# Optimization experiments

Measured on AMD Instinct MI355X. Metric: run time of the kernel, lower is better.

## Reference

```python
import jax, jax.numpy as jnp
import numpy as np


def _conv1d(x, w, pad):
    # torch F.conv1d is cross-correlation; so is lax.conv_general_dilated.
    # x: (k, c_in, N), w: (c_out, c_in, K) -> (k, c_out, N + 2*pad - K + 1)
    return jax.lax.conv_general_dilated(
        x, w, window_strides=(1,), padding=[(pad, pad)],
        dimension_numbers=("NCH", "OIH", "NCH"))


def setup_inputs() -> dict:
    key = jax.random.key(0)
    k1, k2, k3, k4, k5 = jax.random.split(key, 5)
    k_b, c_out, c_in, N, m = 4, 64, 8, 4096, 8
    z_real = jax.random.normal(k1, (k_b, c_in, N), dtype=jnp.float32)
    z_imag = jax.random.normal(k2, (k_b, c_in, N), dtype=jnp.float32)
    A = jax.random.uniform(k3, (c_out, c_in, 1), jnp.float32, 0.75, 1.25)
    beta = jax.random.uniform(k4, (c_out, c_in, 1), jnp.float32, -np.pi, np.pi)
    bias = jax.random.uniform(k5, (c_out, 1), jnp.float32, -0.1, 0.1)
    return {"z_real": z_real, "z_imag": z_imag, "A": A, "beta": beta,
            "bias": bias, "m": m}


def reference(z_real, z_imag, A, beta, bias, m):
    k_b, c_in, N = z_real.shape
    am = abs(int(m))
    ker = N // (2 * am)  # self.ker_size

    # Complex harmonic kernel: |A| * exp(i*(beta + 2*pi*m*phi/N))
    phi = jnp.arange(ker, dtype=jnp.float32)
    ang = beta + (2.0 * jnp.pi * m / N) * phi  # (c_out, c_in, ker)
    absA = jnp.abs(A)
    wr = absA * jnp.cos(ang)
    wi = absA * jnp.sin(ang)

    # Complex conv via 4 real convs: (zr + i zi) * (wr + i wi)
    rr = _conv1d(z_real, wr, ker)
    ii = _conv1d(z_imag, wi, ker)
    ri = _conv1d(z_real, wi, ker)
    ir = _conv1d(z_imag, wr, ker)
    zraw_r = rr - ii  # (k, c_out, N + ker + 1)
    zraw_i = ri + ir

    # Aliasing fold: gather shifted copies, mask out-of-range, alternate sign.
    n = jnp.arange(-2 * am + 1, 2 * am + 1, dtype=jnp.int32)  # (4|m|,)
    mu = jnp.arange(N, dtype=jnp.int32)[:, None]              # (N, 1)
    ind = mu + ker * n                                        # (N, 4|m|)
    cond = ((ind > 0) & (ind < N + ker)).astype(jnp.float32)
    ind = jnp.clip(ind, 0, N + ker)
    menos_1 = (-1.0) ** (1.0 + n.astype(jnp.float32))         # alternating sign
    sign = cond * menos_1                                     # (N, 4|m|)

    gr = zraw_r[:, :, ind]  # (k, c_out, N, 4|m|)
    gi = zraw_i[:, :, ind]
    sr = jnp.einsum("kcnm,nm->kcn", gr, sign)
    si = jnp.einsum("kcnm,nm->kcn", gi, sign)

    # activation: sigmoid(|z| + bias) * z / (|z| + 1e-5)
    mag = jnp.sqrt(sr * sr + si * si)
    gate = jax.nn.sigmoid(mag + bias) / (mag + 1e-5)
    return gate * sr, gate * si
```

## Files before the change

### kernel.cpp

```cpp
#include <hip/hip_runtime.h>
#include <math.h>


#define KB   4
#define COUT 64
#define CIN  8
#define NN   4096
#define INV_N (1.0f / 4096.0f)
#define INV_2PI 0.15915494309189535f

__global__ void f_reduce_kernel(const float* __restrict__ zr,
                                const float* __restrict__ zi,
                                const int* __restrict__ m_ptr,
                                float* __restrict__ F) {
    const int pair = blockIdx.x;
    const int tid  = threadIdx.x;
    const int m    = *m_ptr;
    const float4* xr = (const float4*)(zr + pair * NN);
    const float4* xi = (const float4*)(zi + pair * NN);

    float fcr = 0.f, fsr = 0.f, fci = 0.f, fsi = 0.f;
    #pragma unroll
    for (int it = 0; it < NN / 1024; ++it) {
        int vidx = it * 256 + tid;
        float4 vr = xr[vidx];
        float4 vi = xi[vidx];
        int t0 = vidx * 4;
        #pragma unroll
        for (int j = 0; j < 4; ++j) {
            int r = (m * (t0 + j)) & (NN - 1);
            float rev = (float)r * INV_N;
            float s = __builtin_amdgcn_sinf(rev);
            float c = __builtin_amdgcn_cosf(rev);
            float a = (&vr.x)[j], b = (&vi.x)[j];
            fcr += a * c;  fsr += a * s;
            fci += b * c;  fsi += b * s;
        }
    }
    #pragma unroll
    for (int off = 32; off > 0; off >>= 1) {
        fcr += __shfl_down(fcr, off);
        fsr += __shfl_down(fsr, off);
        fci += __shfl_down(fci, off);
        fsi += __shfl_down(fsi, off);
    }
    __shared__ float red[4][4];
    int wave = tid >> 6, lane = tid & 63;
    if (lane == 0) {
        red[wave][0] = fcr; red[wave][1] = fsr;
        red[wave][2] = fci; red[wave][3] = fsi;
    }
    __syncthreads();
    if (tid == 0) {
        F[pair * 4 + 0] = red[0][0] + red[1][0] + red[2][0] + red[3][0];
        F[pair * 4 + 1] = red[0][1] + red[1][1] + red[2][1] + red[3][1];
        F[pair * 4 + 2] = red[0][2] + red[1][2] + red[2][2] + red[3][2];
        F[pair * 4 + 3] = red[0][3] + red[1][3] + red[2][3] + red[3][3];
    }
}

__global__ void out_kernel(const float* __restrict__ A,
                           const float* __restrict__ beta,
                           const float* __restrict__ bias,
                           const int* __restrict__ m_ptr,
                           const float* __restrict__ F,
                           float* __restrict__ out) {
    const int blk = blockIdx.x;
    const int b = blk >> 6, o = blk & (COUT - 1);
    const int m = *m_ptr;

    float Gr = 0.f, Hr = 0.f, Gi = 0.f, Hi = 0.f;
    #pragma unroll
    for (int i = 0; i < CIN; ++i) {
        float a  = fabsf(A[o * CIN + i]);
        float rb = beta[o * CIN + i] * INV_2PI;
        float sb = __builtin_amdgcn_sinf(rb);
        float cb = __builtin_amdgcn_cosf(rb);
        float P = a * cb, Q = a * sb;
        const float* f = F + (b * CIN + i) * 4;
        float Fcr = f[0], Fsr = f[1], Fci = f[2], Fsi = f[3];
        Gr += -P * Fcr + Q * Fsr + Q * Fci + P * Fsi;
        Hr += -P * Fsr - Q * Fcr + Q * Fsi - P * Fci;
        Gi += -Q * Fcr - P * Fsr - P * Fci + Q * Fsi;
        Hi +=  P * Fcr - Q * Fsr - Q * Fci - P * Fsi;
    }
    const float bo = bias[o];
    const int base = blk << 12;
    const int half = KB * COUT * NN;

    #pragma unroll
    for (int k = 0; k < NN / 256; ++k) {
        int mu = threadIdx.x + k * 256;
        int r = (m * mu) & (NN - 1);
        float rev = (float)r * INV_N;
        float smu = __builtin_amdgcn_sinf(rev);
        float cmu = __builtin_amdgcn_cosf(rev);
        float sr = -(cmu * Gr + smu * Hr);
        float si = -(cmu * Gi + smu * Hi);
        float mag = sqrtf(sr * sr + si * si);
        float gate = 1.0f / (1.0f + __expf(-(mag + bo))) / (mag + 1e-5f);
        out[base + mu]        = gate * sr;
        out[half + base + mu] = gate * si;
    }
}

extern "C" void kernel_launch(void* const* d_in, const int* in_sizes, int n_in,
                              void* d_out, int out_size, void* d_ws, size_t ws_size,
                              hipStream_t stream) {
    const float* z_real = (const float*)d_in[0];
    const float* z_imag = (const float*)d_in[1];
    const float* A      = (const float*)d_in[2];
    const float* beta   = (const float*)d_in[3];
    const float* bias   = (const float*)d_in[4];
    const int*   m_ptr  = (const int*)d_in[5];
    float* out = (float*)d_out;
    float* F   = (float*)d_ws;

    f_reduce_kernel<<<KB * CIN, 256, 0, stream>>>(z_real, z_imag, m_ptr, F);
    out_kernel<<<KB * COUT, 256, 0, stream>>>(A, beta, bias, m_ptr, F, out);
}
```

Baseline: 70.69 us.

## Fuse Fourier reduction and output into one kernel with complex-combined accumulators

Merges the two kernels into a single launch. Each output block recomputes the per-channel complex Fourier coefficient of its batch over all input channels, then reduces the A/beta-weighted sum across the block. The math is recast as a single complex coefficient, so the gate magnitude becomes a per-block constant and the per-element sqrt/exp/divide leave the output loop. The cost is redundant work: every one of the 64 output channels per batch rereads the batch's input (L2-resident) and recomputes the reductions.

```diff
diff --git a/kernel.cpp b/kernel.cpp
--- a/kernel.cpp
+++ b/kernel.cpp
@@ -6,70 +6,57 @@
 #define COUT 64
 #define CIN  8
 #define NN   4096
-#define INV_N (1.0f / 4096.0f)
+#define INV_N   (1.0f / 4096.0f)
 #define INV_2PI 0.15915494309189535f
 
-__global__ void f_reduce_kernel(const float* __restrict__ zr,
-                                const float* __restrict__ zi,
-                                const int* __restrict__ m_ptr,
-                                float* __restrict__ F) {
-    const int pair = blockIdx.x;
-    const int tid  = threadIdx.x;
-    const int m    = *m_ptr;
-    const float4* xr = (const float4*)(zr + pair * NN);
-    const float4* xi = (const float4*)(zi + pair * NN);
+__global__ __launch_bounds__(256) void fused_kernel(
+    const float* __restrict__ zr,
+    const float* __restrict__ zi,
+    const float* __restrict__ A,
+    const float* __restrict__ beta,
+    const float* __restrict__ bias,
+    const int* __restrict__ m_ptr,
+    float* __restrict__ out)
+{
+    const int blk = blockIdx.x;
+    const int b   = blk >> 6;
+    const int o   = blk & (COUT - 1);
+    const int tid = threadIdx.x;
+    const int m   = *m_ptr;
 
-    float fcr = 0.f, fsr = 0.f, fci = 0.f, fsi = 0.f;
+    float cre[CIN], cim[CIN];
+    #pragma unroll
+    for (int i = 0; i < CIN; ++i) { cre[i] = 0.f; cim[i] = 0.f; }
+
+    const float4* xr0 = (const float4*)(zr + b * CIN * NN);
+    const float4* xi0 = (const float4*)(zi + b * CIN * NN);
+
     #pragma unroll
     for (int it = 0; it < NN / 1024; ++it) {
-        int vidx = it * 256 + tid;
-        float4 vr = xr[vidx];
-        float4 vi = xi[vidx];
-        int t0 = vidx * 4;
+        const int vidx = it * 256 + tid;
+        const int t0   = vidx * 4;
+        float sv[4], cv[4];
         #pragma unroll
         for (int j = 0; j < 4; ++j) {
             int r = (m * (t0 + j)) & (NN - 1);
             float rev = (float)r * INV_N;
-            float s = __builtin_amdgcn_sinf(rev);
-            float c = __builtin_amdgcn_cosf(rev);
-            float a = (&vr.x)[j], b = (&vi.x)[j];
-            fcr += a * c;  fsr += a * s;
-            fci += b * c;  fsi += b * s;
+            sv[j] = __builtin_amdgcn_sinf(rev);
+            cv[j] = __builtin_amdgcn_cosf(rev);
+        }
+        #pragma unroll
+        for (int i = 0; i < CIN; ++i) {
+            float4 vr = xr0[i * (NN / 4) + vidx];
+            float4 vi = xi0[i * (NN / 4) + vidx];
+            #pragma unroll
+            for (int j = 0; j < 4; ++j) {
+                float a = (&vr.x)[j], bb = (&vi.x)[j];
+                cre[i] += a * cv[j] - bb * sv[j];
+                cim[i] += a * sv[j] + bb * cv[j];
+            }
         }
     }
-    #pragma unroll
-    for (int off = 32; off > 0; off >>= 1) {
-        fcr += __shfl_down(fcr, off);
-        fsr += __shfl_down(fsr, off);
-        fci += __shfl_down(fci, off);
-        fsi += __shfl_down(fsi, off);
-    }
-    __shared__ float red[4][4];
-    int wave = tid >> 6, lane = tid & 63;
-    if (lane == 0) {
-        red[wave][0] = fcr; red[wave][1] = fsr;
-        red[wave][2] = fci; red[wave][3] = fsi;
-    }
-    __syncthreads();
-    if (tid == 0) {
-        F[pair * 4 + 0] = red[0][0] + red[1][0] + red[2][0] + red[3][0];
-        F[pair * 4 + 1] = red[0][1] + red[1][1] + red[2][1] + red[3][1];
-        F[pair * 4 + 2] = red[0][2] + red[1][2] + red[2][2] + red[3][2];
-        F[pair * 4 + 3] = red[0][3] + red[1][3] + red[2][3] + red[3][3];
-    }
-}
 
-__global__ void out_kernel(const float* __restrict__ A,
-                           const float* __restrict__ beta,
-                           const float* __restrict__ bias,
-                           const int* __restrict__ m_ptr,
-                           const float* __restrict__ F,
-                           float* __restrict__ out) {
-    const int blk = blockIdx.x;
-    const int b = blk >> 6, o = blk & (COUT - 1);
-    const int m = *m_ptr;
-
-    float Gr = 0.f, Hr = 0.f, Gi = 0.f, Hi = 0.f;
+    float Sre = 0.f, Sim = 0.f;
     #pragma unroll
     for (int i = 0; i < CIN; ++i) {
         float a  = fabsf(A[o * CIN + i]);
@@ -77,28 +64,37 @@
         float sb = __builtin_amdgcn_sinf(rb);
         float cb = __builtin_amdgcn_cosf(rb);
         float P = a * cb, Q = a * sb;
-        const float* f = F + (b * CIN + i) * 4;
-        float Fcr = f[0], Fsr = f[1], Fci = f[2], Fsi = f[3];
-        Gr += -P * Fcr + Q * Fsr + Q * Fci + P * Fsi;
-        Hr += -P * Fsr - Q * Fcr + Q * Fsi - P * Fci;
-        Gi += -Q * Fcr - P * Fsr - P * Fci + Q * Fsi;
-        Hi +=  P * Fcr - Q * Fsr - Q * Fci - P * Fsi;
+        Sre += -P * cre[i] + Q * cim[i];
+        Sim += -Q * cre[i] - P * cim[i];
     }
-    const float bo = bias[o];
+
+    #pragma unroll
+    for (int off = 32; off > 0; off >>= 1) {
+        Sre += __shfl_down(Sre, off);
+        Sim += __shfl_down(Sim, off);
+    }
+    __shared__ float red[4][2];
+    const int wave = tid >> 6, lane = tid & 63;
+    if (lane == 0) { red[wave][0] = Sre; red[wave][1] = Sim; }
+    __syncthreads();
+    const float Gr = red[0][0] + red[1][0] + red[2][0] + red[3][0];
+    const float Hr = red[0][1] + red[1][1] + red[2][1] + red[3][1];
+
+    const float mag  = sqrtf(Gr * Gr + Hr * Hr);
+    const float x    = mag + bias[o];
+    const float gate = 1.0f / ((1.0f + __expf(-x)) * (mag + 1e-5f));
+
     const int base = blk << 12;
     const int half = KB * COUT * NN;
-
     #pragma unroll
     for (int k = 0; k < NN / 256; ++k) {
-        int mu = threadIdx.x + k * 256;
+        int mu = tid + k * 256;
         int r = (m * mu) & (NN - 1);
         float rev = (float)r * INV_N;
         float smu = __builtin_amdgcn_sinf(rev);
         float cmu = __builtin_amdgcn_cosf(rev);
         float sr = -(cmu * Gr + smu * Hr);
-        float si = -(cmu * Gi + smu * Hi);
-        float mag = sqrtf(sr * sr + si * si);
-        float gate = 1.0f / (1.0f + __expf(-(mag + bo))) / (mag + 1e-5f);
+        float si = smu * Gr - cmu * Hr;
         out[base + mu]        = gate * sr;
         out[half + base + mu] = gate * si;
     }
@@ -114,8 +110,7 @@
     const float* bias   = (const float*)d_in[4];
     const int*   m_ptr  = (const int*)d_in[5];
     float* out = (float*)d_out;
-    float* F   = (float*)d_ws;
 
-    f_reduce_kernel<<<KB * CIN, 256, 0, stream>>>(z_real, z_imag, m_ptr, F);
-    out_kernel<<<KB * COUT, 256, 0, stream>>>(A, beta, bias, m_ptr, F, out);
+    fused_kernel<<<KB * COUT, 256, 0, stream>>>(z_real, z_imag, A, beta, bias,
+                                                m_ptr, out);
 }
```

New measurement: 70.64 us. About the same (-0.1%).
